# Performance work log

Measured on AMD Instinct MI355X. Metric: run time of the kernel, lower is better.

The kernel has to match this reference:

```python
import jax, jax.numpy as jnp
import numpy as np
from jax import lax
import math

KS = 7  # attention kernel size
PAD = 3


def conv2d(x, w, b, pad):
    y = lax.conv_general_dilated(x, w, (1, 1), [(pad, pad), (pad, pad)],
                                 dimension_numbers=('NCHW', 'OIHW', 'NCHW'))
    return y + b[None, :, None, None]


def unfold(x):
    # x: [B, C, H, W] -> [B, C, KS*KS, H, W], matching nn.Unfold channel-major order
    B, C, H, W = x.shape
    xp = jnp.pad(x, ((0, 0), (0, 0), (PAD, PAD), (PAD, PAD)))
    patches = [xp[:, :, i:i + H, j:j + W] for i in range(KS) for j in range(KS)]
    return jnp.stack(patches, axis=2)


def setup_inputs() -> dict:
    key = jax.random.key(0)
    ks = jax.random.split(key, 12)
    B, H, W = 1, 256, 256
    s = lambda fan: 1.0 / np.sqrt(fan)
    inp = {
        'x': jax.random.normal(ks[0], (B, 6, H, W), jnp.float32),
        'w0': jax.random.normal(ks[1], (48, 3, 3, 3), jnp.float32) * s(3 * 9),
        'b0': jnp.zeros((48,), jnp.float32),
        'w1': jax.random.normal(ks[2], (48, 48, 3, 3), jnp.float32) * s(48 * 9),
        'b1': jnp.zeros((48,), jnp.float32),
        'w2': jax.random.normal(ks[3], (48, 48, 3, 3), jnp.float32) * s(48 * 9),
        'b2': jnp.zeros((48,), jnp.float32),
        'w3': jax.random.normal(ks[4], (24, 48, 3, 3), jnp.float32) * s(48 * 9),
        'b3': jnp.zeros((24,), jnp.float32),
        'skip_w': jax.random.normal(ks[5], (24, 3, 1, 1), jnp.float32) * s(3),
        'skip_b': jnp.zeros((24,), jnp.float32),
        'q_w': jax.random.normal(ks[6], (24, 24, 1, 1), jnp.float32) * s(24),
        'q_b': jnp.zeros((24,), jnp.float32),
        'k_w': jax.random.normal(ks[7], (24, 24, 1, 1), jnp.float32) * s(24),
        'k_b': jnp.zeros((24,), jnp.float32),
        'v_w': jax.random.normal(ks[8], (24, 24, 1, 1), jnp.float32) * s(24),
        'v_b': jnp.zeros((24,), jnp.float32),
    }
    return inp


def reference(x, w0, b0, w1, b1, w2, b2, w3, b3, skip_w, skip_b,
              q_w, q_b, k_w, k_b, v_w, v_b):
    def submodel(t):
        h = jax.nn.relu(conv2d(t, w0, b0, 1))
        h = jax.nn.relu(conv2d(h, w1, b1, 1))
        h = jax.nn.relu(conv2d(h, w2, b2, 1))
        h = jax.nn.relu(conv2d(h, w3, b3, 1))
        return h + conv2d(t, skip_w, skip_b, 0)

    xa, xb = jnp.split(x, 2, axis=1)  # [B,3,H,W] each
    a = submodel(xa)                  # [B,24,H,W]
    b = submodel(xb)

    Q = conv2d(b, q_w, q_b, 0)        # [B,24,H,W]
    K = unfold(conv2d(a, k_w, k_b, 0))  # [B,24,49,H,W]
    V = unfold(conv2d(a, v_w, v_b, 0))  # [B,24,49,H,W]

    C = Q.shape[1]
    A = jnp.einsum('bchw,bcphw->bphw', Q, K) / math.sqrt(C)
    A = jax.nn.softmax(A, axis=1)     # softmax over 49 local positions
    y = jnp.einsum('bphw,bcphw->bchw', A, V)
    return jnp.concatenate([y + a, b], axis=1)  # [B,48,H,W]
```

## Files before the change

### kernel.cpp

```cpp
#include <hip/hip_runtime.h>
#include <math.h>

#define HH 256
#define WW 256
#define NN (HH * WW)

typedef _Float16 f16;
typedef _Float16 f16x8 __attribute__((ext_vector_type(8)));
typedef _Float16 f16x4 __attribute__((ext_vector_type(4)));
typedef _Float16 f16x2 __attribute__((ext_vector_type(2)));
typedef float f32x4 __attribute__((ext_vector_type(4)));

__global__ __launch_bounds__(256) void xh_convert(const float* __restrict__ x,
                                                  f16* __restrict__ xh) {
  int p = blockIdx.x * 256 + threadIdx.x;
  int z = p >= NN;
  int q = p - z * NN;
  const float* xz = x + (size_t)z * 3 * NN;
  f16x4 v;
  v[0] = (f16)xz[q];
  v[1] = (f16)xz[NN + q];
  v[2] = (f16)xz[2 * NN + q];
  v[3] = (f16)0.f;
  *(f16x4*)(xh + (size_t)p * 4) = v;
}

__global__ __launch_bounds__(256) void repack_frags(
    const float* __restrict__ w0, const float* __restrict__ w1,
    const float* __restrict__ w2, const float* __restrict__ w3,
    f16* __restrict__ bf) {
  const int O1 = 1536, O2 = O1 + 27648, O3 = O2 + 27648;
  int e = blockIdx.x * 256 + threadIdx.x;
  if (e >= 75264) return;
  const float* w;
  int COUT, idx, mode;
  if (e < O1)      { w = w0; COUT = 48; idx = e;      mode = 0; }
  else if (e < O2) { w = w1; COUT = 48; idx = e - O1; mode = 1; }
  else if (e < O3) { w = w2; COUT = 48; idx = e - O2; mode = 1; }
  else             { w = w3; COUT = 24; idx = e - O3; mode = 1; }
  int j = idx & 7;
  int lane = (idx >> 3) & 63;
  int rest = idx >> 9;
  int n = lane & 15, quad = lane >> 4;
  float val = 0.f;
  if (mode == 0) {
    int nt = rest;
    int k = quad * 8 + j;
    int cout = nt * 16 + n;
    if (k < 27) {
      int tap = k / 3, ci = k - tap * 3;
      val = w[(cout * 3 + ci) * 9 + tap];
    }
  } else {
    int kc = rest & 1;
    int tap = (rest >> 1) % 9;
    int nt = (rest >> 1) / 9;
    int ci = kc * 32 + quad * 8 + j;
    int cout = nt * 16 + n;
    if (ci < 48 && cout < COUT) val = w[(cout * 48 + ci) * 9 + tap];
  }
  bf[e] = (f16)val;
}

__global__ __launch_bounds__(256, 2) void conv0_gemm(
    const f16* __restrict__ xh, const f16* __restrict__ bf0,
    const float* __restrict__ bias, f16* __restrict__ outh) {
  extern __shared__ char smem[];
  const int tid = threadIdx.x;
  const int lane = tid & 63, wave = tid >> 6;
  const int n = lane & 15, quad = lane >> 4;
  const int bx = blockIdx.x * 16, by = blockIdx.y * 16, z = blockIdx.z;
  const f16* xz = xh + (size_t)z * NN * 4;

  {
    int p = tid, y = p >> 4, xcol = p & 15;
    int gy = by + y, gx = bx + xcol;
    f16* row = (f16*)(smem + p * 80);
#pragma unroll
    for (int tap = 0; tap < 9; ++tap) {
      int dy = tap / 3, dx = tap - (tap / 3) * 3;
      int sy = gy + dy - 1, sx = gx + dx - 1;
      f16 c0 = (f16)0.f, c1 = c0, c2 = c0;
      if (sy >= 0 && sy < HH && sx >= 0 && sx < WW) {
        const f16* s = xz + ((size_t)sy * WW + sx) * 4;
        c0 = s[0]; c1 = s[1]; c2 = s[2];
      }
      row[tap * 3 + 0] = c0;
      row[tap * 3 + 1] = c1;
      row[tap * 3 + 2] = c2;
    }
#pragma unroll
    for (int k = 27; k < 32; ++k) row[k] = (f16)0.f;
  }
  __syncthreads();

  f32x4 acc[4][3];
#pragma unroll
  for (int nt = 0; nt < 3; ++nt) {
    float bv = bias[nt * 16 + n];
#pragma unroll
    for (int i = 0; i < 4; ++i) acc[i][nt] = (f32x4){bv, bv, bv, bv};
  }
  f16x8 B[3];
#pragma unroll
  for (int nt = 0; nt < 3; ++nt)
    B[nt] = *(const f16x8*)(bf0 + (nt * 64 + lane) * 8);
#pragma unroll
  for (int i = 0; i < 4; ++i) {
    int r = wave * 4 + i;
    f16x8 a = *(const f16x8*)(smem + (r * 16 + n) * 80 + quad * 16);
#pragma unroll
    for (int nt = 0; nt < 3; ++nt)
      acc[i][nt] =
          __builtin_amdgcn_mfma_f32_16x16x32_f16(a, B[nt], acc[i][nt], 0, 0, 0);
  }

  f16* oz = outh + (size_t)z * NN * 48;
#pragma unroll
  for (int i = 0; i < 4; ++i) {
    int y = by + wave * 4 + i;
#pragma unroll
    for (int nt = 0; nt < 3; ++nt)
#pragma unroll
      for (int reg = 0; reg < 4; ++reg)
        oz[((size_t)y * WW + bx + quad * 4 + reg) * 48 + nt * 16 + n] =
            (f16)fmaxf(acc[i][nt][reg], 0.f);
  }
}

template <int NT, int COUT, bool FUSE>
__global__ __launch_bounds__(256, 2) void gemm_conv(
    const f16* __restrict__ in, const f16* __restrict__ bfr,
    const float* __restrict__ bias, f16* __restrict__ outh,
    float* __restrict__ outf, const float* __restrict__ xsrc,
    const float* __restrict__ skw, const float* __restrict__ skb) {
  extern __shared__ char smem[];
  float* xt = (float*)(smem + 324 * 144);
  const int tid = threadIdx.x;
  const int lane = tid & 63, wave = tid >> 6;
  const int n = lane & 15, quad = lane >> 4;
  const int bx = blockIdx.x * 16, by = blockIdx.y * 16, z = blockIdx.z;
  const f16* inz = in + (size_t)z * NN * 48;

  for (int p = tid; p < 324; p += 256) {
    int yy = p / 18, xx = p - yy * 18;
    int gy = by + yy - 1, gx = bx + xx - 1;
    float4* dst = (float4*)(smem + p * 144);
    if (gy >= 0 && gy < HH && gx >= 0 && gx < WW) {
      const float4* s = (const float4*)(inz + ((size_t)gy * WW + gx) * 48);
      float4 a0 = s[0], a1 = s[1], a2 = s[2], a3 = s[3], a4 = s[4], a5 = s[5];
      dst[0] = a0; dst[1] = a1; dst[2] = a2;
      dst[3] = a3; dst[4] = a4; dst[5] = a5;
      dst[6] = make_float4(0, 0, 0, 0);
      dst[7] = make_float4(0, 0, 0, 0);
    } else {
      float4 zz = make_float4(0, 0, 0, 0);
#pragma unroll
      for (int c = 0; c < 8; ++c) dst[c] = zz;
    }
  }
  if (FUSE) {
    for (int i = tid; i < 768; i += 256) {
      int c = i >> 8, p = i & 255;
      xt[i] = xsrc[(size_t)z * 3 * NN + c * NN + (by + (p >> 4)) * WW + bx +
                   (p & 15)];
    }
  }
  __syncthreads();

  f32x4 acc[4][NT];
#pragma unroll
  for (int nt = 0; nt < NT; ++nt) {
    int cc = nt * 16 + n;
    float bv = (cc < COUT) ? bias[cc] : 0.f;
#pragma unroll
    for (int i = 0; i < 4; ++i) acc[i][nt] = (f32x4){bv, bv, bv, bv};
  }

  const int r0 = wave * 4;
#pragma unroll
  for (int tap = 0; tap < 9; ++tap) {
    const int dy = tap / 3, dx = tap - dy * 3;
    f16x8 B[2][NT];
#pragma unroll
    for (int kc = 0; kc < 2; ++kc)
#pragma unroll
      for (int nt = 0; nt < NT; ++nt)
        B[kc][nt] =
            *(const f16x8*)(bfr + (((nt * 9 + tap) * 2 + kc) * 64 + lane) * 8);
#pragma unroll
    for (int i = 0; i < 4; ++i) {
      const int p = (r0 + i + dy) * 18 + (n + dx);
      const char* ap = smem + p * 144;
      f16x8 a0 = *(const f16x8*)(ap + quad * 16);
      f16x8 a1 = *(const f16x8*)(ap + 64 + quad * 16);
#pragma unroll
      for (int nt = 0; nt < NT; ++nt)
        acc[i][nt] = __builtin_amdgcn_mfma_f32_16x16x32_f16(a0, B[0][nt],
                                                            acc[i][nt], 0, 0, 0);
#pragma unroll
      for (int nt = 0; nt < NT; ++nt)
        acc[i][nt] = __builtin_amdgcn_mfma_f32_16x16x32_f16(a1, B[1][nt],
                                                            acc[i][nt], 0, 0, 0);
    }
  }

  if (!FUSE) {
    f16* oz = outh + (size_t)z * NN * 48;
#pragma unroll
    for (int i = 0; i < 4; ++i) {
      int y = by + r0 + i;
#pragma unroll
      for (int nt = 0; nt < NT; ++nt)
#pragma unroll
        for (int reg = 0; reg < 4; ++reg)
          oz[((size_t)y * WW + bx + quad * 4 + reg) * 48 + nt * 16 + n] =
              (f16)fmaxf(acc[i][nt][reg], 0.f);
    }
  } else {
    float* oz = outf + (size_t)z * 24 * NN;
#pragma unroll
    for (int i = 0; i < 4; ++i) {
      int y = by + r0 + i;
#pragma unroll
      for (int nt = 0; nt < NT; ++nt) {
        int cc = nt * 16 + n;
        if (cc < 24) {
          float s0 = skw[cc * 3 + 0], s1 = skw[cc * 3 + 1],
                s2 = skw[cc * 3 + 2], sb0 = skb[cc];
          f32x4 o;
#pragma unroll
          for (int reg = 0; reg < 4; ++reg) {
            int pl = (r0 + i) * 16 + quad * 4 + reg;
            float sk = sb0 + s0 * xt[pl] + s1 * xt[256 + pl] + s2 * xt[512 + pl];
            o[reg] = fmaxf(acc[i][nt][reg], 0.f) + sk;
          }
          *(f32x4*)(oz + (size_t)cc * NN + (size_t)y * WW + bx + quad * 4) = o;
        }
      }
    }
  }
}

__global__ __launch_bounds__(256) void qkv_kernel(
    const float* __restrict__ a, const float* __restrict__ b,
    const float* __restrict__ qw, const float* __restrict__ qb,
    const float* __restrict__ kw, const float* __restrict__ kb,
    const float* __restrict__ vw, const float* __restrict__ vb,
    f16* __restrict__ Qh, f16* __restrict__ KVh) {
  const int p = blockIdx.x * 256 + threadIdx.x;
  float av[24], bv[24];
#pragma unroll
  for (int c = 0; c < 24; ++c) {
    av[c] = a[c * NN + p];
    bv[c] = b[c * NN + p];
  }
  f16 qo[24], ko[24], vo[24];
#pragma unroll
  for (int co = 0; co < 24; ++co) {
    float sq = qb[co], sk = kb[co], sv = vb[co];
#pragma unroll
    for (int ci = 0; ci < 24; ++ci) {
      sq = fmaf(bv[ci], qw[co * 24 + ci], sq);
      sk = fmaf(av[ci], kw[co * 24 + ci], sk);
      sv = fmaf(av[ci], vw[co * 24 + ci], sv);
    }
    qo[co] = (f16)sq;
    ko[co] = (f16)sk;
    vo[co] = (f16)sv;
  }
#pragma unroll
  for (int t = 0; t < 3; ++t)
    *(f16x8*)(Qh + (size_t)p * 24 + t * 8) = *(f16x8*)(qo + t * 8);
#pragma unroll
  for (int t = 0; t < 3; ++t)
    *(f16x8*)(KVh + (size_t)p * 48 + t * 8) = *(f16x8*)(ko + t * 8);
#pragma unroll
  for (int t = 0; t < 3; ++t)
    *(f16x8*)(KVh + (size_t)p * 48 + 24 + t * 8) = *(f16x8*)(vo + t * 8);
}

__device__ inline float dot8(f16x8 a, f16x8 b, float acc) {
#if __has_builtin(__builtin_amdgcn_fdot2)
#pragma unroll
  for (int i = 0; i < 4; ++i)
    acc = __builtin_amdgcn_fdot2(
        __builtin_shufflevector(a, a, 0, 1) ,
        __builtin_shufflevector(b, b, 0, 1), acc, false);
  return acc;
#else
#pragma unroll
  for (int i = 0; i < 8; ++i) acc += (float)a[i] * (float)b[i];
  return acc;
#endif
}

__device__ inline float dot8p(f16x8 a, f16x8 b, float acc) {
#if __has_builtin(__builtin_amdgcn_fdot2)
  acc = __builtin_amdgcn_fdot2(__builtin_shufflevector(a, a, 0, 1),
                               __builtin_shufflevector(b, b, 0, 1), acc, false);
  acc = __builtin_amdgcn_fdot2(__builtin_shufflevector(a, a, 2, 3),
                               __builtin_shufflevector(b, b, 2, 3), acc, false);
  acc = __builtin_amdgcn_fdot2(__builtin_shufflevector(a, a, 4, 5),
                               __builtin_shufflevector(b, b, 4, 5), acc, false);
  acc = __builtin_amdgcn_fdot2(__builtin_shufflevector(a, a, 6, 7),
                               __builtin_shufflevector(b, b, 6, 7), acc, false);
  return acc;
#else
#pragma unroll
  for (int i = 0; i < 8; ++i) acc += (float)a[i] * (float)b[i];
  return acc;
#endif
}

__global__ __launch_bounds__(256, 3) void attn_kernel(
    const f16* __restrict__ Qh, const f16* __restrict__ KVh,
    const float* __restrict__ ab, float* __restrict__ out) {
  extern __shared__ f16 kv[];
  const int tid = threadIdx.x;
  const int bx = blockIdx.x * 32, by = blockIdx.y * 8;

  for (int idx = tid; idx < 3192; idx += 256) {
    int row = idx / 228;
    int rem = idx - row * 228;
    int pxl = rem / 6;
    int c = rem - pxl * 6;
    int gy = by + row - 3, gx = bx + pxl - 3;
    f16x8 v = {};
    if (gy >= 0 && gy < HH && gx >= 0 && gx < WW)
      v = *(const f16x8*)(KVh + ((size_t)(gy * WW + gx)) * 48 + c * 8);
    *(f16x8*)(kv + (row * 38 + pxl) * 56 + c * 8) = v;
  }
  __syncthreads();

  const int xl = tid & 31, yl = tid >> 5;
  const int p = (by + yl) * WW + bx + xl;

  f16x8 q0 = *(const f16x8*)(Qh + (size_t)p * 24);
  f16x8 q1 = *(const f16x8*)(Qh + (size_t)p * 24 + 8);
  f16x8 q2 = *(const f16x8*)(Qh + (size_t)p * 24 + 16);

  float s[49];
#pragma unroll
  for (int pp = 0; pp < 49; ++pp) {
    int dy = pp / 7, dx = pp - dy * 7;
    const f16* base = kv + ((yl + dy) * 38 + xl + dx) * 56;
    f16x8 k0 = *(const f16x8*)(base);
    f16x8 k1 = *(const f16x8*)(base + 8);
    f16x8 k2 = *(const f16x8*)(base + 16);
    float d = 0.f;
    d = dot8p(q0, k0, d);
    d = dot8p(q1, k1, d);
    d = dot8p(q2, k2, d);
    s[pp] = d * 0.20412414523193154f;
  }

  float m = s[0];
#pragma unroll
  for (int pp = 1; pp < 49; ++pp) m = fmaxf(m, s[pp]);
  float den = 0.f;
#pragma unroll
  for (int pp = 0; pp < 49; ++pp) {
    float e = __expf(s[pp] - m);
    s[pp] = e;
    den += e;
  }
  const float inv = 1.f / den;

  f16x8 y0 = {}, y1 = {}, y2 = {};
#pragma unroll
  for (int pp = 0; pp < 49; ++pp) {
    int dy = pp / 7, dx = pp - dy * 7;
    const f16* base = kv + ((yl + dy) * 38 + xl + dx) * 56 + 24;
    f16 wh = (f16)(s[pp] * inv);
    f16x8 w8 = {wh, wh, wh, wh, wh, wh, wh, wh};
    f16x8 v0 = *(const f16x8*)(base);
    f16x8 v1 = *(const f16x8*)(base + 8);
    f16x8 v2 = *(const f16x8*)(base + 16);
    y0 = v0 * w8 + y0;
    y1 = v1 * w8 + y1;
    y2 = v2 * w8 + y2;
  }

#pragma unroll
  for (int c = 0; c < 8; ++c)
    out[(size_t)c * NN + p] = (float)y0[c] + ab[(size_t)c * NN + p];
#pragma unroll
  for (int c = 0; c < 8; ++c)
    out[(size_t)(8 + c) * NN + p] = (float)y1[c] + ab[(size_t)(8 + c) * NN + p];
#pragma unroll
  for (int c = 0; c < 8; ++c)
    out[(size_t)(16 + c) * NN + p] =
        (float)y2[c] + ab[(size_t)(16 + c) * NN + p];
#pragma unroll
  for (int c = 24; c < 48; ++c)
    out[(size_t)c * NN + p] = ab[(size_t)c * NN + p];
}

extern "C" void kernel_launch(void* const* d_in, const int* in_sizes, int n_in,
                              void* d_out, int out_size, void* d_ws,
                              size_t ws_size, hipStream_t stream) {
  const float* x = (const float*)d_in[0];
  const float* w0 = (const float*)d_in[1];
  const float* b0 = (const float*)d_in[2];
  const float* w1 = (const float*)d_in[3];
  const float* b1 = (const float*)d_in[4];
  const float* w2 = (const float*)d_in[5];
  const float* b2 = (const float*)d_in[6];
  const float* w3 = (const float*)d_in[7];
  const float* b3 = (const float*)d_in[8];
  const float* sw = (const float*)d_in[9];
  const float* sb = (const float*)d_in[10];
  const float* qw = (const float*)d_in[11];
  const float* qb = (const float*)d_in[12];
  const float* kw = (const float*)d_in[13];
  const float* kb = (const float*)d_in[14];
  const float* vw = (const float*)d_in[15];
  const float* vb = (const float*)d_in[16];
  float* out = (float*)d_out;
  float* ws = (float*)d_ws;

  float* AB = ws;
  f16* Qh = (f16*)(ws + (size_t)48 * NN);
  f16* KVh = (f16*)(ws + (size_t)60 * NN);
  f16* ACT0 = (f16*)(ws + (size_t)120 * NN);
  f16* ACT1 = (f16*)(ws + (size_t)168 * NN);
  f16* XH = (f16*)(ws + (size_t)216 * NN);
  f16* BF = (f16*)(ws + (size_t)220 * NN);

  xh_convert<<<dim3(512), dim3(256), 0, stream>>>(x, XH);
  repack_frags<<<dim3(294), dim3(256), 0, stream>>>(w0, w1, w2, w3, BF);

  dim3 cgrd(16, 16, 2);
  conv0_gemm<<<cgrd, dim3(256), 256 * 80, stream>>>(XH, BF, b0, ACT0);
  gemm_conv<3, 48, false><<<cgrd, dim3(256), 324 * 144, stream>>>(
      ACT0, BF + 1536, b1, ACT1, nullptr, nullptr, nullptr, nullptr);
  gemm_conv<3, 48, false><<<cgrd, dim3(256), 324 * 144, stream>>>(
      ACT1, BF + 29184, b2, ACT0, nullptr, nullptr, nullptr, nullptr);
  gemm_conv<2, 24, true><<<cgrd, dim3(256), 324 * 144 + 3072, stream>>>(
      ACT0, BF + 56832, b3, nullptr, AB, x, sw, sb);

  qkv_kernel<<<dim3(256), dim3(256), 0, stream>>>(AB, AB + 24 * NN, qw, qb, kw,
                                                  kb, vw, vb, Qh, KVh);

  attn_kernel<<<dim3(8, 32), dim3(256), 532 * 112, stream>>>(Qh, KVh, AB, out);
}
```

Measured before the change: 184.9 us.

## Store submodel outputs as pixel-major fp16 and compute QKV projections with MFMA

The fused last conv now writes a and b as fp16 in a pixel-major layout padded to 32 channels, where it used to write fp32 channel-major planes. The 1x1 Q/K/V projections move from per-thread scalar FMAs onto MFMA instructions, and their weights are repacked into fragments by the existing repack kernel. The attention epilogue reads the fp16 residuals as vectors, and the Q loads are hoisted ahead of the shared-memory fill. This cuts intermediate memory traffic and ALU work, at the cost of fp16 rounding on the residual paths and on the b half of the output.

After: 159.3 us. 13.9% less time.

```diff
diff --git a/kernel.cpp b/kernel.cpp
--- a/kernel.cpp
+++ b/kernel.cpp
@@ -8,7 +8,6 @@
 typedef _Float16 f16;
 typedef _Float16 f16x8 __attribute__((ext_vector_type(8)));
 typedef _Float16 f16x4 __attribute__((ext_vector_type(4)));
-typedef _Float16 f16x2 __attribute__((ext_vector_type(2)));
 typedef float f32x4 __attribute__((ext_vector_type(4)));
 
 __global__ __launch_bounds__(256) void xh_convert(const float* __restrict__ x,
@@ -28,36 +27,50 @@
 __global__ __launch_bounds__(256) void repack_frags(
     const float* __restrict__ w0, const float* __restrict__ w1,
     const float* __restrict__ w2, const float* __restrict__ w3,
-    f16* __restrict__ bf) {
-  const int O1 = 1536, O2 = O1 + 27648, O3 = O2 + 27648;
+    const float* __restrict__ qw, const float* __restrict__ kw,
+    const float* __restrict__ vw, f16* __restrict__ bf) {
+  const int O1 = 1536, O2 = O1 + 27648, O3 = O2 + 27648, OQ = O3 + 18432;
   int e = blockIdx.x * 256 + threadIdx.x;
-  if (e >= 75264) return;
-  const float* w;
-  int COUT, idx, mode;
-  if (e < O1)      { w = w0; COUT = 48; idx = e;      mode = 0; }
-  else if (e < O2) { w = w1; COUT = 48; idx = e - O1; mode = 1; }
-  else if (e < O3) { w = w2; COUT = 48; idx = e - O2; mode = 1; }
-  else             { w = w3; COUT = 24; idx = e - O3; mode = 1; }
-  int j = idx & 7;
-  int lane = (idx >> 3) & 63;
-  int rest = idx >> 9;
-  int n = lane & 15, quad = lane >> 4;
+  if (e >= OQ + 3072) return;
   float val = 0.f;
-  if (mode == 0) {
-    int nt = rest;
-    int k = quad * 8 + j;
-    int cout = nt * 16 + n;
-    if (k < 27) {
-      int tap = k / 3, ci = k - tap * 3;
-      val = w[(cout * 3 + ci) * 9 + tap];
-    }
+  if (e >= OQ) {
+    int idx = e - OQ;
+    int mat = idx >> 10;
+    int r = idx & 1023;
+    int nt = r >> 9;
+    int lane = (r >> 3) & 63;
+    int j = r & 7;
+    int n = lane & 15, quad = lane >> 4;
+    int ci = quad * 8 + j, co = nt * 16 + n;
+    const float* w = (mat == 0) ? qw : (mat == 1) ? kw : vw;
+    if (ci < 24 && co < 24) val = w[co * 24 + ci];
   } else {
-    int kc = rest & 1;
-    int tap = (rest >> 1) % 9;
-    int nt = (rest >> 1) / 9;
-    int ci = kc * 32 + quad * 8 + j;
-    int cout = nt * 16 + n;
-    if (ci < 48 && cout < COUT) val = w[(cout * 48 + ci) * 9 + tap];
+    const float* w;
+    int COUT, idx, mode;
+    if (e < O1)      { w = w0; COUT = 48; idx = e;      mode = 0; }
+    else if (e < O2) { w = w1; COUT = 48; idx = e - O1; mode = 1; }
+    else if (e < O3) { w = w2; COUT = 48; idx = e - O2; mode = 1; }
+    else             { w = w3; COUT = 24; idx = e - O3; mode = 1; }
+    int j = idx & 7;
+    int lane = (idx >> 3) & 63;
+    int rest = idx >> 9;
+    int n = lane & 15, quad = lane >> 4;
+    if (mode == 0) {
+      int nt = rest;
+      int k = quad * 8 + j;
+      int cout = nt * 16 + n;
+      if (k < 27) {
+        int tap = k / 3, ci = k - tap * 3;
+        val = w[(cout * 3 + ci) * 9 + tap];
+      }
+    } else {
+      int kc = rest & 1;
+      int tap = (rest >> 1) % 9;
+      int nt = (rest >> 1) / 9;
+      int ci = kc * 32 + quad * 8 + j;
+      int cout = nt * 16 + n;
+      if (ci < 48 && cout < COUT) val = w[(cout * 48 + ci) * 9 + tap];
+    }
   }
   bf[e] = (f16)val;
 }
@@ -132,8 +145,8 @@
 __global__ __launch_bounds__(256, 2) void gemm_conv(
     const f16* __restrict__ in, const f16* __restrict__ bfr,
     const float* __restrict__ bias, f16* __restrict__ outh,
-    float* __restrict__ outf, const float* __restrict__ xsrc,
-    const float* __restrict__ skw, const float* __restrict__ skb) {
+    const float* __restrict__ xsrc, const float* __restrict__ skw,
+    const float* __restrict__ skb) {
   extern __shared__ char smem[];
   float* xt = (float*)(smem + 324 * 144);
   const int tid = threadIdx.x;
@@ -218,81 +231,111 @@
               (f16)fmaxf(acc[i][nt][reg], 0.f);
     }
   } else {
-    float* oz = outf + (size_t)z * 24 * NN;
+    f16* oz = outh + (size_t)z * NN * 32;
 #pragma unroll
     for (int i = 0; i < 4; ++i) {
       int y = by + r0 + i;
 #pragma unroll
       for (int nt = 0; nt < NT; ++nt) {
         int cc = nt * 16 + n;
+        float s0 = 0.f, s1 = 0.f, s2 = 0.f, sb0 = 0.f;
         if (cc < 24) {
-          float s0 = skw[cc * 3 + 0], s1 = skw[cc * 3 + 1],
-                s2 = skw[cc * 3 + 2], sb0 = skb[cc];
-          f32x4 o;
-#pragma unroll
-          for (int reg = 0; reg < 4; ++reg) {
+          s0 = skw[cc * 3 + 0];
+          s1 = skw[cc * 3 + 1];
+          s2 = skw[cc * 3 + 2];
+          sb0 = skb[cc];
+        }
+#pragma unroll
+        for (int reg = 0; reg < 4; ++reg) {
+          float v = 0.f;
+          if (cc < 24) {
             int pl = (r0 + i) * 16 + quad * 4 + reg;
             float sk = sb0 + s0 * xt[pl] + s1 * xt[256 + pl] + s2 * xt[512 + pl];
-            o[reg] = fmaxf(acc[i][nt][reg], 0.f) + sk;
+            v = fmaxf(acc[i][nt][reg], 0.f) + sk;
           }
-          *(f32x4*)(oz + (size_t)cc * NN + (size_t)y * WW + bx + quad * 4) = o;
+          oz[((size_t)(y * WW + bx + quad * 4 + reg)) * 32 + cc] = (f16)v;
         }
       }
     }
   }
 }
 
-__global__ __launch_bounds__(256) void qkv_kernel(
-    const float* __restrict__ a, const float* __restrict__ b,
-    const float* __restrict__ qw, const float* __restrict__ qb,
-    const float* __restrict__ kw, const float* __restrict__ kb,
-    const float* __restrict__ vw, const float* __restrict__ vb,
-    f16* __restrict__ Qh, f16* __restrict__ KVh) {
-  const int p = blockIdx.x * 256 + threadIdx.x;
-  float av[24], bv[24];
-#pragma unroll
-  for (int c = 0; c < 24; ++c) {
-    av[c] = a[c * NN + p];
-    bv[c] = b[c * NN + p];
-  }
-  f16 qo[24], ko[24], vo[24];
-#pragma unroll
-  for (int co = 0; co < 24; ++co) {
-    float sq = qb[co], sk = kb[co], sv = vb[co];
-#pragma unroll
-    for (int ci = 0; ci < 24; ++ci) {
-      sq = fmaf(bv[ci], qw[co * 24 + ci], sq);
-      sk = fmaf(av[ci], kw[co * 24 + ci], sk);
-      sv = fmaf(av[ci], vw[co * 24 + ci], sv);
-    }
-    qo[co] = (f16)sq;
-    ko[co] = (f16)sk;
-    vo[co] = (f16)sv;
-  }
-#pragma unroll
-  for (int t = 0; t < 3; ++t)
-    *(f16x8*)(Qh + (size_t)p * 24 + t * 8) = *(f16x8*)(qo + t * 8);
-#pragma unroll
-  for (int t = 0; t < 3; ++t)
-    *(f16x8*)(KVh + (size_t)p * 48 + t * 8) = *(f16x8*)(ko + t * 8);
-#pragma unroll
-  for (int t = 0; t < 3; ++t)
-    *(f16x8*)(KVh + (size_t)p * 48 + 24 + t * 8) = *(f16x8*)(vo + t * 8);
-}
-
-__device__ inline float dot8(f16x8 a, f16x8 b, float acc) {
-#if __has_builtin(__builtin_amdgcn_fdot2)
-#pragma unroll
-  for (int i = 0; i < 4; ++i)
-    acc = __builtin_amdgcn_fdot2(
-        __builtin_shufflevector(a, a, 0, 1) ,
-        __builtin_shufflevector(b, b, 0, 1), acc, false);
-  return acc;
-#else
-#pragma unroll
-  for (int i = 0; i < 8; ++i) acc += (float)a[i] * (float)b[i];
-  return acc;
-#endif
+__global__ __launch_bounds__(256) void qkv_mfma(
+    const f16* __restrict__ ABh, const f16* __restrict__ bf,
+    const float* __restrict__ qb, const float* __restrict__ kb,
+    const float* __restrict__ vb, f16* __restrict__ Qh,
+    f16* __restrict__ KVh) {
+  const int OQ = 75264;
+  const int tid = threadIdx.x;
+  const int lane = tid & 63, wave = tid >> 6;
+  const int n = lane & 15, quad = lane >> 4;
+  const int z = blockIdx.y;
+  const f16* src = ABh + (size_t)z * NN * 32;
+
+  if (z == 1) {
+    f16x8 QF[2];
+#pragma unroll
+    for (int nt = 0; nt < 2; ++nt)
+      QF[nt] = *(const f16x8*)(bf + OQ + (nt * 64 + lane) * 8);
+    float qbias[2];
+#pragma unroll
+    for (int nt = 0; nt < 2; ++nt) {
+      int cc = nt * 16 + n;
+      qbias[nt] = (cc < 24) ? qb[cc] : 0.f;
+    }
+#pragma unroll
+    for (int t = 0; t < 4; ++t) {
+      int T = blockIdx.x * 16 + wave * 4 + t;
+      size_t p0 = (size_t)T * 16;
+      f16x8 a8 = *(const f16x8*)(src + p0 * 32 + n * 32 + quad * 8);
+#pragma unroll
+      for (int nt = 0; nt < 2; ++nt) {
+        f32x4 acc = {qbias[nt], qbias[nt], qbias[nt], qbias[nt]};
+        acc = __builtin_amdgcn_mfma_f32_16x16x32_f16(a8, QF[nt], acc, 0, 0, 0);
+        int cc = nt * 16 + n;
+        if (cc < 24) {
+#pragma unroll
+          for (int reg = 0; reg < 4; ++reg)
+            Qh[(p0 + quad * 4 + reg) * 24 + cc] = (f16)acc[reg];
+        }
+      }
+    }
+  } else {
+    f16x8 KF[2], VF[2];
+#pragma unroll
+    for (int nt = 0; nt < 2; ++nt) {
+      KF[nt] = *(const f16x8*)(bf + OQ + 1024 + (nt * 64 + lane) * 8);
+      VF[nt] = *(const f16x8*)(bf + OQ + 2048 + (nt * 64 + lane) * 8);
+    }
+    float kbias[2], vbias[2];
+#pragma unroll
+    for (int nt = 0; nt < 2; ++nt) {
+      int cc = nt * 16 + n;
+      kbias[nt] = (cc < 24) ? kb[cc] : 0.f;
+      vbias[nt] = (cc < 24) ? vb[cc] : 0.f;
+    }
+#pragma unroll
+    for (int t = 0; t < 4; ++t) {
+      int T = blockIdx.x * 16 + wave * 4 + t;
+      size_t p0 = (size_t)T * 16;
+      f16x8 a8 = *(const f16x8*)(src + p0 * 32 + n * 32 + quad * 8);
+#pragma unroll
+      for (int nt = 0; nt < 2; ++nt) {
+        f32x4 ak = {kbias[nt], kbias[nt], kbias[nt], kbias[nt]};
+        f32x4 av = {vbias[nt], vbias[nt], vbias[nt], vbias[nt]};
+        ak = __builtin_amdgcn_mfma_f32_16x16x32_f16(a8, KF[nt], ak, 0, 0, 0);
+        av = __builtin_amdgcn_mfma_f32_16x16x32_f16(a8, VF[nt], av, 0, 0, 0);
+        int cc = nt * 16 + n;
+        if (cc < 24) {
+#pragma unroll
+          for (int reg = 0; reg < 4; ++reg) {
+            KVh[(p0 + quad * 4 + reg) * 48 + cc] = (f16)ak[reg];
+            KVh[(p0 + quad * 4 + reg) * 48 + 24 + cc] = (f16)av[reg];
+          }
+        }
+      }
+    }
+  }
 }
 
 __device__ inline float dot8p(f16x8 a, f16x8 b, float acc) {
@@ -315,10 +358,16 @@
 
 __global__ __launch_bounds__(256, 3) void attn_kernel(
     const f16* __restrict__ Qh, const f16* __restrict__ KVh,
-    const float* __restrict__ ab, float* __restrict__ out) {
+    const f16* __restrict__ ABh, float* __restrict__ out) {
   extern __shared__ f16 kv[];
   const int tid = threadIdx.x;
   const int bx = blockIdx.x * 32, by = blockIdx.y * 8;
+  const int xl = tid & 31, yl = tid >> 5;
+  const int p = (by + yl) * WW + bx + xl;
+
+  f16x8 q0 = *(const f16x8*)(Qh + (size_t)p * 24);
+  f16x8 q1 = *(const f16x8*)(Qh + (size_t)p * 24 + 8);
+  f16x8 q2 = *(const f16x8*)(Qh + (size_t)p * 24 + 16);
 
   for (int idx = tid; idx < 3192; idx += 256) {
     int row = idx / 228;
@@ -332,13 +381,6 @@
     *(f16x8*)(kv + (row * 38 + pxl) * 56 + c * 8) = v;
   }
   __syncthreads();
-
-  const int xl = tid & 31, yl = tid >> 5;
-  const int p = (by + yl) * WW + bx + xl;
-
-  f16x8 q0 = *(const f16x8*)(Qh + (size_t)p * 24);
-  f16x8 q1 = *(const f16x8*)(Qh + (size_t)p * 24 + 8);
-  f16x8 q2 = *(const f16x8*)(Qh + (size_t)p * 24 + 16);
 
   float s[49];
 #pragma unroll
@@ -382,19 +424,23 @@
     y2 = v2 * w8 + y2;
   }
 
-#pragma unroll
-  for (int c = 0; c < 8; ++c)
-    out[(size_t)c * NN + p] = (float)y0[c] + ab[(size_t)c * NN + p];
-#pragma unroll
-  for (int c = 0; c < 8; ++c)
-    out[(size_t)(8 + c) * NN + p] = (float)y1[c] + ab[(size_t)(8 + c) * NN + p];
-#pragma unroll
-  for (int c = 0; c < 8; ++c)
-    out[(size_t)(16 + c) * NN + p] =
-        (float)y2[c] + ab[(size_t)(16 + c) * NN + p];
-#pragma unroll
-  for (int c = 24; c < 48; ++c)
-    out[(size_t)c * NN + p] = ab[(size_t)c * NN + p];
+  const f16* ah = ABh + (size_t)p * 32;
+  const f16* bh = ABh + (size_t)NN * 32 + (size_t)p * 32;
+  f16x8 a0 = *(const f16x8*)(ah);
+  f16x8 a1 = *(const f16x8*)(ah + 8);
+  f16x8 a2 = *(const f16x8*)(ah + 16);
+  f16x8 b0 = *(const f16x8*)(bh);
+  f16x8 b1 = *(const f16x8*)(bh + 8);
+  f16x8 b2 = *(const f16x8*)(bh + 16);
+#pragma unroll
+  for (int c = 0; c < 8; ++c) {
+    out[(size_t)c * NN + p] = (float)y0[c] + (float)a0[c];
+    out[(size_t)(8 + c) * NN + p] = (float)y1[c] + (float)a1[c];
+    out[(size_t)(16 + c) * NN + p] = (float)y2[c] + (float)a2[c];
+    out[(size_t)(24 + c) * NN + p] = (float)b0[c];
+    out[(size_t)(32 + c) * NN + p] = (float)b1[c];
+    out[(size_t)(40 + c) * NN + p] = (float)b2[c];
+  }
 }
 
 extern "C" void kernel_launch(void* const* d_in, const int* in_sizes, int n_in,
@@ -420,28 +466,29 @@
   float* out = (float*)d_out;
   float* ws = (float*)d_ws;
 
-  float* AB = ws;
-  f16* Qh = (f16*)(ws + (size_t)48 * NN);
-  f16* KVh = (f16*)(ws + (size_t)60 * NN);
-  f16* ACT0 = (f16*)(ws + (size_t)120 * NN);
-  f16* ACT1 = (f16*)(ws + (size_t)168 * NN);
-  f16* XH = (f16*)(ws + (size_t)216 * NN);
-  f16* BF = (f16*)(ws + (size_t)220 * NN);
+  f16* Qh = (f16*)(ws);
+  f16* KVh = (f16*)(ws + (size_t)12 * NN);
+  f16* ABh = (f16*)(ws + (size_t)36 * NN);
+  f16* ACT0 = (f16*)(ws + (size_t)68 * NN);
+  f16* ACT1 = (f16*)(ws + (size_t)116 * NN);
+  f16* XH = (f16*)(ws + (size_t)164 * NN);
+  f16* BF = (f16*)(ws + (size_t)168 * NN);
 
   xh_convert<<<dim3(512), dim3(256), 0, stream>>>(x, XH);
-  repack_frags<<<dim3(294), dim3(256), 0, stream>>>(w0, w1, w2, w3, BF);
+  repack_frags<<<dim3(306), dim3(256), 0, stream>>>(w0, w1, w2, w3, qw, kw, vw,
+                                                    BF);
 
   dim3 cgrd(16, 16, 2);
   conv0_gemm<<<cgrd, dim3(256), 256 * 80, stream>>>(XH, BF, b0, ACT0);
   gemm_conv<3, 48, false><<<cgrd, dim3(256), 324 * 144, stream>>>(
-      ACT0, BF + 1536, b1, ACT1, nullptr, nullptr, nullptr, nullptr);
+      ACT0, BF + 1536, b1, ACT1, nullptr, nullptr, nullptr);
   gemm_conv<3, 48, false><<<cgrd, dim3(256), 324 * 144, stream>>>(
-      ACT1, BF + 29184, b2, ACT0, nullptr, nullptr, nullptr, nullptr);
+      ACT1, BF + 29184, b2, ACT0, nullptr, nullptr, nullptr);
   gemm_conv<2, 24, true><<<cgrd, dim3(256), 324 * 144 + 3072, stream>>>(
-      ACT0, BF + 56832, b3, nullptr, AB, x, sw, sb);
-
-  qkv_kernel<<<dim3(256), dim3(256), 0, stream>>>(AB, AB + 24 * NN, qw, qb, kw,
-                                                  kb, vw, vb, Qh, KVh);
-
-  attn_kernel<<<dim3(8, 32), dim3(256), 532 * 112, stream>>>(Qh, KVh, AB, out);
-}
+      ACT0, BF + 56832, b3, ABh, x, sw, sb);
+
+  qkv_mfma<<<dim3(256, 2), dim3(256), 0, stream>>>(ABh, BF, qb, kb, vb, Qh,
+                                                   KVh);
+
+  attn_kernel<<<dim3(8, 32), dim3(256), 532 * 112, stream>>>(Qh, KVh, ABh, out);
+}
```
